# Kernel tuning notes

Hardware: AMD Instinct MI355X
Metric: run time of the kernel (lower is better)

The kernel has to match this reference:

```python
import jax, jax.numpy as jnp
import numpy as np

N_NODES = 100000
N_EDGES = 1600000
N_GRAPHS = 512
IN_DIM = 128
HID = 128


def setup_inputs() -> dict:
    key = jax.random.key(0)
    ks = jax.random.split(key, 8)
    x = jax.random.normal(ks[0], (N_NODES, IN_DIM), dtype=jnp.float32)
    edge_index = jax.random.randint(ks[1], (2, N_EDGES), 0, N_NODES, dtype=jnp.int64)
    batch = jnp.sort(jax.random.randint(ks[2], (N_NODES,), 0, N_GRAPHS, dtype=jnp.int64))
    s1 = 1.0 / np.sqrt(IN_DIM)
    s2 = 1.0 / np.sqrt(HID)
    W1 = jax.random.normal(ks[3], (IN_DIM, HID), dtype=jnp.float32) * s1
    b1 = jnp.zeros((HID,), dtype=jnp.float32)
    W2 = jax.random.normal(ks[4], (HID, HID), dtype=jnp.float32) * s2
    b2 = jnp.zeros((HID,), dtype=jnp.float32)
    Wp = jax.random.normal(ks[5], (HID, 1), dtype=jnp.float32) * s2
    bp = jnp.zeros((1,), dtype=jnp.float32)
    return {"x": x, "edge_index": edge_index, "batch": batch,
            "W1": W1, "b1": b1, "W2": W2, "b2": b2, "Wp": Wp, "bp": bp}


def _gcn_conv(x, W, b, src, dst, deg_inv_sqrt):
    # PyG GCNConv: linear transform, then normalized scatter-add (self-loops
    # already appended to src/dst), then bias.
    h = x @ W                                   # [N, H]
    norm = deg_inv_sqrt[src] * deg_inv_sqrt[dst]  # [E+N]
    msg = h[src] * norm[:, None]                # gather + scale
    out = jax.ops.segment_sum(msg, dst, num_segments=N_NODES)
    return out + b


def reference(x, edge_index, batch, W1, b1, W2, b2, Wp, bp):
    # Add self-loops once; degree (with self-loops) over target nodes.
    si = jnp.arange(N_NODES, dtype=edge_index.dtype)
    src = jnp.concatenate([edge_index[0], si])
    dst = jnp.concatenate([edge_index[1], si])
    ones = jnp.ones(src.shape[0], dtype=x.dtype)
    deg = jax.ops.segment_sum(ones, dst, num_segments=N_NODES)
    deg_inv_sqrt = jnp.where(deg > 0, jax.lax.rsqrt(jnp.maximum(deg, 1.0)), 0.0)

    h = jax.nn.relu(_gcn_conv(x, W1, b1, src, dst, deg_inv_sqrt))  # dropout = identity (eval)
    h = jax.nn.relu(_gcn_conv(h, W2, b2, src, dst, deg_inv_sqrt))

    # global_mean_pool over graph ids
    sums = jax.ops.segment_sum(h, batch, num_segments=N_GRAPHS)
    cnts = jax.ops.segment_sum(jnp.ones(N_NODES, dtype=h.dtype), batch, num_segments=N_GRAPHS)
    pooled = sums / jnp.maximum(cnts, 1.0)[:, None]               # [G, H]

    return (pooled @ Wp + bp).squeeze(-1)                          # [G]
```

## Files before the change

kernel.cpp:

```cpp
#include <hip/hip_runtime.h>
#include <hip/hip_bf16.h>

#define NN 100000
#define NG 512
#define H  128

typedef _Float16 half8 __attribute__((ext_vector_type(8)));
typedef _Float16 half4v __attribute__((ext_vector_type(4)));
typedef float f32x4 __attribute__((ext_vector_type(4)));

__global__ __launch_bounds__(256) void k_hist(const int* __restrict__ dst,
                                              int* __restrict__ deg, int E) {
    int e = blockIdx.x * 256 + threadIdx.x;
    if (e < E) atomicAdd(&deg[dst[e]], 1);
}

__global__ __launch_bounds__(256) void k_scan_block(const int* __restrict__ deg,
                                                    int* __restrict__ rowptr,
                                                    int* __restrict__ bsum, int n) {
    __shared__ int s[256];
    int tid = threadIdx.x;
    int i = blockIdx.x * 256 + tid;
    int v = (i < n) ? deg[i] : 0;
    s[tid] = v;
    __syncthreads();
    #pragma unroll
    for (int off = 1; off < 256; off <<= 1) {
        int t = (tid >= off) ? s[tid - off] : 0;
        __syncthreads();
        s[tid] += t;
        __syncthreads();
    }
    if (i < n) rowptr[i] = s[tid] - v;
    if (tid == 255) bsum[blockIdx.x] = s[255];
}

__global__ __launch_bounds__(512) void k_scan_top(int* __restrict__ bsum, int nb) {
    __shared__ int s[512];
    int tid = threadIdx.x;
    int v = (tid < nb) ? bsum[tid] : 0;
    s[tid] = v;
    __syncthreads();
    #pragma unroll
    for (int off = 1; off < 512; off <<= 1) {
        int t = (tid >= off) ? s[tid - off] : 0;
        __syncthreads();
        s[tid] += t;
        __syncthreads();
    }
    if (tid < nb) bsum[tid] = s[tid] - v;
}

__global__ __launch_bounds__(256) void k_scan_fin(int* __restrict__ rowptr,
                                                  const int* __restrict__ bsum,
                                                  const int* __restrict__ deg,
                                                  int* __restrict__ cursor,
                                                  float* __restrict__ dinv,
                                                  int n, int E) {
    int i = blockIdx.x * 256 + threadIdx.x;
    if (i >= n) return;
    int r = rowptr[i] + bsum[i >> 8];
    rowptr[i] = r;
    cursor[i] = r;
    dinv[i] = rsqrtf((float)deg[i] + 1.0f);
    if (i == 0) rowptr[n] = E;
}

__global__ __launch_bounds__(256) void k_fill(const int* __restrict__ src,
                                              const int* __restrict__ dst,
                                              int* __restrict__ cursor,
                                              int* __restrict__ col, int E) {
    int e = blockIdx.x * 256 + threadIdx.x;
    if (e >= E) return;
    int d = dst[e];
    int pos = atomicAdd(&cursor[d], 1);
    col[pos] = src[e];
}

__global__ __launch_bounds__(256) void k_sortrows(const int* __restrict__ rowptr,
                                                  int* __restrict__ col, int n) {
    int node = blockIdx.x * 4 + (threadIdx.x >> 6);
    int lane = threadIdx.x & 63;
    if (node >= n) return;
    int e0 = rowptr[node], end = rowptr[node + 1];
    int deg = end - e0;
    if (deg <= 1 || deg > 64) return;
    int v = (lane < deg) ? col[e0 + lane] : 0x7fffffff;
    #pragma unroll
    for (int k = 2; k <= 64; k <<= 1) {
        #pragma unroll
        for (int j = k >> 1; j > 0; j >>= 1) {
            int p = __shfl_xor(v, j);
            bool up = ((lane & k) == 0);
            bool keepmin = (((lane & j) == 0) == up);
            v = keepmin ? min(v, p) : max(v, p);
        }
    }
    if (lane < deg) col[e0 + lane] = v;
}

__global__ __launch_bounds__(256) void k_cvt_h(const float* __restrict__ in,
                                               _Float16* __restrict__ out, int n4) {
    int i = blockIdx.x * 256 + threadIdx.x;
    if (i >= n4) return;
    float4 v = ((const float4*)in)[i];
    half4v h;
    h[0] = (_Float16)v.x;
    h[1] = (_Float16)v.y;
    h[2] = (_Float16)v.z;
    h[3] = (_Float16)v.w;
    ((half4v*)out)[i] = h;
}

#define LDA 136
__global__ __launch_bounds__(256) void gemm_mfma(const _Float16* __restrict__ A,
                                                 const float* __restrict__ W,
                                                 const float* __restrict__ scale,
                                                 _Float16* __restrict__ C, int n) {
    __shared__ _Float16 As[64 * LDA];
    __shared__ _Float16 Wt[128 * LDA];
    const int tid = threadIdx.x;
    const int row0 = blockIdx.x * 64;

    #pragma unroll
    for (int i = 0; i < 4; ++i) {
        int f = i * 256 + tid;
        int r = f >> 4, c8 = f & 15;
        int gr = row0 + r;
        half8 v;
        #pragma unroll
        for (int j = 0; j < 8; ++j) v[j] = (_Float16)0.0f;
        if (gr < n) v = ((const half8*)(A + (size_t)gr * H))[c8];
        *((half8*)(As + r * LDA + c8 * 8)) = v;
    }
    #pragma unroll
    for (int i = 0; i < 16; ++i) {
        int f = i * 256 + tid;
        int k = f >> 5, c4 = f & 31;
        float4 v = ((const float4*)(W + (size_t)k * H))[c4];
        Wt[(c4 * 4 + 0) * LDA + k] = (_Float16)v.x;
        Wt[(c4 * 4 + 1) * LDA + k] = (_Float16)v.y;
        Wt[(c4 * 4 + 2) * LDA + k] = (_Float16)v.z;
        Wt[(c4 * 4 + 3) * LDA + k] = (_Float16)v.w;
    }
    __syncthreads();

    const int w = tid >> 6;
    const int lane = tid & 63;
    const int l16 = lane & 15, quad = lane >> 4;
    f32x4 acc[8] = {};
    const _Float16* aBase = As + (w * 16 + l16) * LDA + quad * 8;
    const _Float16* bBase = Wt + l16 * LDA + quad * 8;
    #pragma unroll
    for (int kk = 0; kk < 4; ++kk) {
        half8 af = *((const half8*)(aBase + kk * 32));
        #pragma unroll
        for (int nt = 0; nt < 8; ++nt) {
            half8 bf = *((const half8*)(bBase + nt * 16 * LDA + kk * 32));
            acc[nt] = __builtin_amdgcn_mfma_f32_16x16x32_f16(af, bf, acc[nt], 0, 0, 0);
        }
    }
    #pragma unroll
    for (int r = 0; r < 4; ++r) {
        int R = row0 + w * 16 + quad * 4 + r;
        if (R < n) {
            float sc = scale[R];
            _Float16* crow = C + (size_t)R * H + l16;
            #pragma unroll
            for (int nt = 0; nt < 8; ++nt)
                crow[nt * 16] = (_Float16)(acc[nt][r] * sc);
        }
    }
}

__device__ __forceinline__ void gather_rows_h(const half8* __restrict__ t8,
                                              const int* __restrict__ col,
                                              int node, int e0, int end,
                                              float acc[8]) {
    const int lane = threadIdx.x & 63;
    const int q = lane >> 4;
    const int l16 = lane & 15;
    float a0[8] = {}, a1[8] = {};
    if (q == 0) {
        half8 v = t8[(size_t)node * 16 + l16];
        #pragma unroll
        for (int i = 0; i < 8; ++i) a0[i] = (float)v[i];
    }
    for (int base = e0; base < end; base += 64) {
        int ce = base + lane;
        int cidx = (ce < end) ? col[ce] : 0;
        int m = min(64, end - base);
        int nf = m >> 2;
        int g = 0;
        for (; g + 2 <= nf; g += 2) {
            int s0 = __shfl(cidx, 4 * g + q);
            int s1 = __shfl(cidx, 4 * g + 4 + q);
            half8 v0 = t8[(size_t)s0 * 16 + l16];
            half8 v1 = t8[(size_t)s1 * 16 + l16];
            #pragma unroll
            for (int i = 0; i < 8; ++i) {
                a0[i] += (float)v0[i];
                a1[i] += (float)v1[i];
            }
        }
        if (g < nf) {
            int s0 = __shfl(cidx, 4 * g + q);
            half8 v0 = t8[(size_t)s0 * 16 + l16];
            #pragma unroll
            for (int i = 0; i < 8; ++i) a0[i] += (float)v0[i];
        }
        int tail = m & 3;
        if (tail) {
            int s = __shfl(cidx, 4 * nf + q);
            if (q < tail) {
                half8 v = t8[(size_t)s * 16 + l16];
                #pragma unroll
                for (int i = 0; i < 8; ++i) a0[i] += (float)v[i];
            }
        }
    }
    #pragma unroll
    for (int i = 0; i < 8; ++i) {
        float t = a0[i] + a1[i];
        t += __shfl_xor(t, 16);
        t += __shfl_xor(t, 32);
        acc[i] = t;
    }
}

__global__ __launch_bounds__(256) void k_gather1(const _Float16* __restrict__ tS,
                                                 const int* __restrict__ rowptr,
                                                 const int* __restrict__ col,
                                                 const float* __restrict__ dinv,
                                                 const float* __restrict__ b,
                                                 _Float16* __restrict__ out, int n) {
    int node = blockIdx.x * 4 + (threadIdx.x >> 6);
    int lane = threadIdx.x & 63;
    int q = lane >> 4, l16 = lane & 15;
    if (node >= n) return;
    int e0 = rowptr[node], end = rowptr[node + 1];
    float acc[8];
    gather_rows_h((const half8*)tS, col, node, e0, end, acc);
    if (q == 0) {
        float dn = dinv[node];
        const float4* b4 = (const float4*)b;
        float4 bb0 = b4[2 * l16], bb1 = b4[2 * l16 + 1];
        half8 hv;
        hv[0] = (_Float16)fmaxf(dn * acc[0] + bb0.x, 0.0f);
        hv[1] = (_Float16)fmaxf(dn * acc[1] + bb0.y, 0.0f);
        hv[2] = (_Float16)fmaxf(dn * acc[2] + bb0.z, 0.0f);
        hv[3] = (_Float16)fmaxf(dn * acc[3] + bb0.w, 0.0f);
        hv[4] = (_Float16)fmaxf(dn * acc[4] + bb1.x, 0.0f);
        hv[5] = (_Float16)fmaxf(dn * acc[5] + bb1.y, 0.0f);
        hv[6] = (_Float16)fmaxf(dn * acc[6] + bb1.z, 0.0f);
        hv[7] = (_Float16)fmaxf(dn * acc[7] + bb1.w, 0.0f);
        ((half8*)out)[(size_t)node * 16 + l16] = hv;
    }
}

__global__ __launch_bounds__(256) void k_gather2(const _Float16* __restrict__ tS,
                                                 const int* __restrict__ rowptr,
                                                 const int* __restrict__ col,
                                                 const float* __restrict__ dinv,
                                                 const float* __restrict__ b,
                                                 const float* __restrict__ Wp,
                                                 const int* __restrict__ batch,
                                                 float* __restrict__ pool,
                                                 float* __restrict__ cnt, int n) {
    int node = blockIdx.x * 4 + (threadIdx.x >> 6);
    int lane = threadIdx.x & 63;
    int l16 = lane & 15;
    if (node >= n) return;
    int e0 = rowptr[node], end = rowptr[node + 1];
    float acc[8];
    gather_rows_h((const half8*)tS, col, node, e0, end, acc);
    float dn = dinv[node];
    const float4* b4 = (const float4*)b;
    const float4* w4 = (const float4*)Wp;
    float4 bb0 = b4[2 * l16], bb1 = b4[2 * l16 + 1];
    float4 wp0 = w4[2 * l16], wp1 = w4[2 * l16 + 1];
    float s = fmaxf(dn * acc[0] + bb0.x, 0.0f) * wp0.x +
              fmaxf(dn * acc[1] + bb0.y, 0.0f) * wp0.y +
              fmaxf(dn * acc[2] + bb0.z, 0.0f) * wp0.z +
              fmaxf(dn * acc[3] + bb0.w, 0.0f) * wp0.w +
              fmaxf(dn * acc[4] + bb1.x, 0.0f) * wp1.x +
              fmaxf(dn * acc[5] + bb1.y, 0.0f) * wp1.y +
              fmaxf(dn * acc[6] + bb1.z, 0.0f) * wp1.z +
              fmaxf(dn * acc[7] + bb1.w, 0.0f) * wp1.w;
    s += __shfl_xor(s, 1);
    s += __shfl_xor(s, 2);
    s += __shfl_xor(s, 4);
    s += __shfl_xor(s, 8);
    if (lane == 0) {
        int g = batch[node];
        atomicAdd(&pool[g], s);
        atomicAdd(&cnt[g], 1.0f);
    }
}

__global__ __launch_bounds__(256) void final_out_kernel(const float* __restrict__ pool,
                                                        const float* __restrict__ cnt,
                                                        const float* __restrict__ bp,
                                                        float* __restrict__ out, int g) {
    int i = blockIdx.x * 256 + threadIdx.x;
    if (i < g) out[i] = pool[i] / fmaxf(cnt[i], 1.0f) + bp[0];
}

extern "C" void kernel_launch(void* const* d_in, const int* in_sizes, int n_in,
                              void* d_out, int out_size, void* d_ws, size_t ws_size,
                              hipStream_t stream) {
    const float* x     = (const float*)d_in[0];
    const int*   ei    = (const int*)d_in[1];
    const int*   batch = (const int*)d_in[2];
    const float* W1    = (const float*)d_in[3];
    const float* b1    = (const float*)d_in[4];
    const float* W2    = (const float*)d_in[5];
    const float* b2    = (const float*)d_in[6];
    const float* Wp    = (const float*)d_in[7];
    const float* bp    = (const float*)d_in[8];
    float* out = (float*)d_out;

    const int E = in_sizes[1] / 2;
    const int* src = ei;
    const int* dst = ei + E;

    const size_t BUFH = (size_t)NN * H * sizeof(_Float16);
    const size_t NI  = 401408;
    char* ws = (char*)d_ws;
    size_t off = 0;
    _Float16* tS  = (_Float16*)(ws + off); off += BUFH;
    _Float16* h1  = (_Float16*)(ws + off); off += BUFH;
    _Float16* xh  = (_Float16*)(ws + off); off += BUFH;
    int*   deg    = (int*)  (ws + off); off += NI;
    int*   rowptr = (int*)  (ws + off); off += NI;
    int*   cursor = (int*)  (ws + off); off += NI;
    float* dinv   = (float*)(ws + off); off += NI;
    int*   col    = (int*)  (ws + off); off += ((size_t)E * 4 + 4095) / 4096 * 4096;
    int*   bsum   = (int*)  (ws + off); off += 4096;
    float* pool   = (float*)(ws + off); off += 2048;
    float* cnt    = (float*)(ws + off); off += 2048;

    const int NB = (NN + 255) / 256;

    hipMemsetAsync(deg, 0, NN * sizeof(int), stream);
    hipMemsetAsync(pool, 0, 4096, stream);
    k_hist<<<(E + 255) / 256, 256, 0, stream>>>(dst, deg, E);
    k_scan_block<<<NB, 256, 0, stream>>>(deg, rowptr, bsum, NN);
    k_scan_top<<<1, 512, 0, stream>>>(bsum, NB);
    k_scan_fin<<<NB, 256, 0, stream>>>(rowptr, bsum, deg, cursor, dinv, NN, E);
    k_fill<<<(E + 255) / 256, 256, 0, stream>>>(src, dst, cursor, col, E);
    k_sortrows<<<(NN + 3) / 4, 256, 0, stream>>>(rowptr, col, NN);

    k_cvt_h<<<(NN * 32 + 255) / 256, 256, 0, stream>>>(x, xh, NN * 32);

    gemm_mfma<<<(NN + 63) / 64, 256, 0, stream>>>(xh, W1, dinv, tS, NN);
    k_gather1<<<(NN + 3) / 4, 256, 0, stream>>>(tS, rowptr, col, dinv, b1, h1, NN);

    gemm_mfma<<<(NN + 63) / 64, 256, 0, stream>>>(h1, W2, dinv, tS, NN);
    k_gather2<<<(NN + 3) / 4, 256, 0, stream>>>(tS, rowptr, col, dinv, b2, Wp,
                                                batch, pool, cnt, NN);

    final_out_kernel<<<(NG + 255) / 256, 256, 0, stream>>>(pool, cnt, bp, out, NG);
}
```

Measured before the change: 704.6 us.

## Fuse fill with GEMM1, fuse gather1 with GEMM2, sort rows in-register

Several kernels are merged. The half-precision conversion of x moves into the first GEMM, which also shares one launch with the CSR fill. The second GEMM is fused into the first aggregation kernel through shared memory, so h1 never goes to global memory. The per-row sort pass is dropped and each gather wave sorts its own neighbor list with a bitonic network. Weight transposition is done once up front instead of in every GEMM block. This removes launches and memory round trips, but it adds redundant sorting work in both gathers and lowers gather parallelism to one 64-node block per workgroup, with each wave looping over 16 nodes serially.

```diff
diff --git a/kernel.cpp b/kernel.cpp
--- a/kernel.cpp
+++ b/kernel.cpp
@@ -6,7 +6,6 @@
 #define H  128
 
 typedef _Float16 half8 __attribute__((ext_vector_type(8)));
-typedef _Float16 half4v __attribute__((ext_vector_type(4)));
 typedef float f32x4 __attribute__((ext_vector_type(4)));
 
 __global__ __launch_bounds__(256) void k_hist(const int* __restrict__ dst,
@@ -66,26 +65,72 @@
     if (i == 0) rowptr[n] = E;
 }
 
-__global__ __launch_bounds__(256) void k_fill(const int* __restrict__ src,
-                                              const int* __restrict__ dst,
-                                              int* __restrict__ cursor,
-                                              int* __restrict__ col, int E) {
-    int e = blockIdx.x * 256 + threadIdx.x;
-    if (e >= E) return;
-    int d = dst[e];
-    int pos = atomicAdd(&cursor[d], 1);
-    col[pos] = src[e];
-}
-
-__global__ __launch_bounds__(256) void k_sortrows(const int* __restrict__ rowptr,
-                                                  int* __restrict__ col, int n) {
-    int node = blockIdx.x * 4 + (threadIdx.x >> 6);
-    int lane = threadIdx.x & 63;
-    if (node >= n) return;
-    int e0 = rowptr[node], end = rowptr[node + 1];
-    int deg = end - e0;
-    if (deg <= 1 || deg > 64) return;
-    int v = (lane < deg) ? col[e0 + lane] : 0x7fffffff;
+__global__ __launch_bounds__(256) void k_wprep(const float* __restrict__ W1,
+                                               const float* __restrict__ W2,
+                                               _Float16* __restrict__ Wt1,
+                                               _Float16* __restrict__ Wt2) {
+    int bb = blockIdx.x;
+    const float* W = (bb < 64) ? W1 : W2;
+    _Float16* Wt = (bb < 64) ? Wt1 : Wt2;
+    int i = (bb & 63) * 256 + threadIdx.x;
+    int k = i >> 7, n = i & 127;
+    Wt[n * 128 + k] = (_Float16)W[i];
+}
+
+__global__ __launch_bounds__(256) void k_fill_gemm1(
+        const int* __restrict__ src, const int* __restrict__ dst,
+        int* __restrict__ cursor, int* __restrict__ col, int E, int nfb,
+        const float* __restrict__ x, const _Float16* __restrict__ Wt1,
+        const float* __restrict__ dinv, _Float16* __restrict__ tS, int n) {
+    if ((int)blockIdx.x < nfb) {
+        int e = blockIdx.x * 256 + threadIdx.x;
+        if (e >= E) return;
+        int d = dst[e];
+        int pos = atomicAdd(&cursor[d], 1);
+        col[pos] = src[e];
+        return;
+    }
+    const int row0 = ((int)blockIdx.x - nfb) * 64;
+    const int tid = threadIdx.x;
+    const int w = tid >> 6, lane = tid & 63;
+    const int l16 = lane & 15, quad = lane >> 4;
+    const int Arow = row0 + w * 16 + l16;
+    f32x4 acc[8] = {};
+    #pragma unroll
+    for (int kk = 0; kk < 4; ++kk) {
+        half8 af;
+        if (Arow < n) {
+            const float* ap = x + (size_t)Arow * H + kk * 32 + quad * 8;
+            float4 a0 = ((const float4*)ap)[0];
+            float4 a1 = ((const float4*)ap)[1];
+            af[0] = (_Float16)a0.x; af[1] = (_Float16)a0.y;
+            af[2] = (_Float16)a0.z; af[3] = (_Float16)a0.w;
+            af[4] = (_Float16)a1.x; af[5] = (_Float16)a1.y;
+            af[6] = (_Float16)a1.z; af[7] = (_Float16)a1.w;
+        } else {
+            #pragma unroll
+            for (int j = 0; j < 8; ++j) af[j] = (_Float16)0.0f;
+        }
+        #pragma unroll
+        for (int nt = 0; nt < 8; ++nt) {
+            half8 bf = *((const half8*)(Wt1 + (nt * 16 + l16) * H + kk * 32 + quad * 8));
+            acc[nt] = __builtin_amdgcn_mfma_f32_16x16x32_f16(af, bf, acc[nt], 0, 0, 0);
+        }
+    }
+    #pragma unroll
+    for (int r = 0; r < 4; ++r) {
+        int R = row0 + w * 16 + quad * 4 + r;
+        if (R < n) {
+            float sc = dinv[R];
+            _Float16* crow = tS + (size_t)R * H + l16;
+            #pragma unroll
+            for (int nt = 0; nt < 8; ++nt)
+                crow[nt * 16] = (_Float16)(acc[nt][r] * sc);
+        }
+    }
+}
+
+__device__ __forceinline__ int bitonic64(int v, int lane) {
     #pragma unroll
     for (int k = 2; k <= 64; k <<= 1) {
         #pragma unroll
@@ -96,81 +141,7 @@
             v = keepmin ? min(v, p) : max(v, p);
         }
     }
-    if (lane < deg) col[e0 + lane] = v;
-}
-
-__global__ __launch_bounds__(256) void k_cvt_h(const float* __restrict__ in,
-                                               _Float16* __restrict__ out, int n4) {
-    int i = blockIdx.x * 256 + threadIdx.x;
-    if (i >= n4) return;
-    float4 v = ((const float4*)in)[i];
-    half4v h;
-    h[0] = (_Float16)v.x;
-    h[1] = (_Float16)v.y;
-    h[2] = (_Float16)v.z;
-    h[3] = (_Float16)v.w;
-    ((half4v*)out)[i] = h;
-}
-
-#define LDA 136
-__global__ __launch_bounds__(256) void gemm_mfma(const _Float16* __restrict__ A,
-                                                 const float* __restrict__ W,
-                                                 const float* __restrict__ scale,
-                                                 _Float16* __restrict__ C, int n) {
-    __shared__ _Float16 As[64 * LDA];
-    __shared__ _Float16 Wt[128 * LDA];
-    const int tid = threadIdx.x;
-    const int row0 = blockIdx.x * 64;
-
-    #pragma unroll
-    for (int i = 0; i < 4; ++i) {
-        int f = i * 256 + tid;
-        int r = f >> 4, c8 = f & 15;
-        int gr = row0 + r;
-        half8 v;
-        #pragma unroll
-        for (int j = 0; j < 8; ++j) v[j] = (_Float16)0.0f;
-        if (gr < n) v = ((const half8*)(A + (size_t)gr * H))[c8];
-        *((half8*)(As + r * LDA + c8 * 8)) = v;
-    }
-    #pragma unroll
-    for (int i = 0; i < 16; ++i) {
-        int f = i * 256 + tid;
-        int k = f >> 5, c4 = f & 31;
-        float4 v = ((const float4*)(W + (size_t)k * H))[c4];
-        Wt[(c4 * 4 + 0) * LDA + k] = (_Float16)v.x;
-        Wt[(c4 * 4 + 1) * LDA + k] = (_Float16)v.y;
-        Wt[(c4 * 4 + 2) * LDA + k] = (_Float16)v.z;
-        Wt[(c4 * 4 + 3) * LDA + k] = (_Float16)v.w;
-    }
-    __syncthreads();
-
-    const int w = tid >> 6;
-    const int lane = tid & 63;
-    const int l16 = lane & 15, quad = lane >> 4;
-    f32x4 acc[8] = {};
-    const _Float16* aBase = As + (w * 16 + l16) * LDA + quad * 8;
-    const _Float16* bBase = Wt + l16 * LDA + quad * 8;
-    #pragma unroll
-    for (int kk = 0; kk < 4; ++kk) {
-        half8 af = *((const half8*)(aBase + kk * 32));
-        #pragma unroll
-        for (int nt = 0; nt < 8; ++nt) {
-            half8 bf = *((const half8*)(bBase + nt * 16 * LDA + kk * 32));
-            acc[nt] = __builtin_amdgcn_mfma_f32_16x16x32_f16(af, bf, acc[nt], 0, 0, 0);
-        }
-    }
-    #pragma unroll
-    for (int r = 0; r < 4; ++r) {
-        int R = row0 + w * 16 + quad * 4 + r;
-        if (R < n) {
-            float sc = scale[R];
-            _Float16* crow = C + (size_t)R * H + l16;
-            #pragma unroll
-            for (int nt = 0; nt < 8; ++nt)
-                crow[nt * 16] = (_Float16)(acc[nt][r] * sc);
-        }
-    }
+    return v;
 }
 
 __device__ __forceinline__ void gather_rows_h(const half8* __restrict__ t8,
@@ -186,9 +157,11 @@
         #pragma unroll
         for (int i = 0; i < 8; ++i) a0[i] = (float)v[i];
     }
+    const bool small = (end - e0) <= 64;
     for (int base = e0; base < end; base += 64) {
         int ce = base + lane;
-        int cidx = (ce < end) ? col[ce] : 0;
+        int cidx = (ce < end) ? col[ce] : 0x7fffffff;
+        if (small) cidx = bitonic64(cidx, lane);
         int m = min(64, end - base);
         int nf = m >> 2;
         int g = 0;
@@ -228,33 +201,67 @@
     }
 }
 
-__global__ __launch_bounds__(256) void k_gather1(const _Float16* __restrict__ tS,
-                                                 const int* __restrict__ rowptr,
-                                                 const int* __restrict__ col,
-                                                 const float* __restrict__ dinv,
-                                                 const float* __restrict__ b,
-                                                 _Float16* __restrict__ out, int n) {
-    int node = blockIdx.x * 4 + (threadIdx.x >> 6);
-    int lane = threadIdx.x & 63;
-    int q = lane >> 4, l16 = lane & 15;
-    if (node >= n) return;
-    int e0 = rowptr[node], end = rowptr[node + 1];
-    float acc[8];
-    gather_rows_h((const half8*)tS, col, node, e0, end, acc);
-    if (q == 0) {
-        float dn = dinv[node];
-        const float4* b4 = (const float4*)b;
-        float4 bb0 = b4[2 * l16], bb1 = b4[2 * l16 + 1];
+#define LDA 136
+__global__ __launch_bounds__(256) void k_gather1f(const _Float16* __restrict__ tS,
+                                                  const int* __restrict__ rowptr,
+                                                  const int* __restrict__ col,
+                                                  const float* __restrict__ dinv,
+                                                  const float* __restrict__ b,
+                                                  const _Float16* __restrict__ Wt2,
+                                                  _Float16* __restrict__ tS2, int n) {
+    __shared__ _Float16 As[64 * LDA];
+    const int tid = threadIdx.x;
+    const int w = tid >> 6, lane = tid & 63;
+    const int q = lane >> 4, l16 = lane & 15, quad = lane >> 4;
+    const int node0 = blockIdx.x * 64;
+    const float4* b4 = (const float4*)b;
+    float4 bb0 = b4[2 * l16], bb1 = b4[2 * l16 + 1];
+
+    for (int i = 0; i < 16; ++i) {
+        int node = node0 + w * 16 + i;
         half8 hv;
-        hv[0] = (_Float16)fmaxf(dn * acc[0] + bb0.x, 0.0f);
-        hv[1] = (_Float16)fmaxf(dn * acc[1] + bb0.y, 0.0f);
-        hv[2] = (_Float16)fmaxf(dn * acc[2] + bb0.z, 0.0f);
-        hv[3] = (_Float16)fmaxf(dn * acc[3] + bb0.w, 0.0f);
-        hv[4] = (_Float16)fmaxf(dn * acc[4] + bb1.x, 0.0f);
-        hv[5] = (_Float16)fmaxf(dn * acc[5] + bb1.y, 0.0f);
-        hv[6] = (_Float16)fmaxf(dn * acc[6] + bb1.z, 0.0f);
-        hv[7] = (_Float16)fmaxf(dn * acc[7] + bb1.w, 0.0f);
-        ((half8*)out)[(size_t)node * 16 + l16] = hv;
+        #pragma unroll
+        for (int j = 0; j < 8; ++j) hv[j] = (_Float16)0.0f;
+        if (node < n) {
+            int e0 = rowptr[node], end = rowptr[node + 1];
+            float acc[8];
+            gather_rows_h((const half8*)tS, col, node, e0, end, acc);
+            float dn = dinv[node];
+            hv[0] = (_Float16)fmaxf(dn * acc[0] + bb0.x, 0.0f);
+            hv[1] = (_Float16)fmaxf(dn * acc[1] + bb0.y, 0.0f);
+            hv[2] = (_Float16)fmaxf(dn * acc[2] + bb0.z, 0.0f);
+            hv[3] = (_Float16)fmaxf(dn * acc[3] + bb0.w, 0.0f);
+            hv[4] = (_Float16)fmaxf(dn * acc[4] + bb1.x, 0.0f);
+            hv[5] = (_Float16)fmaxf(dn * acc[5] + bb1.y, 0.0f);
+            hv[6] = (_Float16)fmaxf(dn * acc[6] + bb1.z, 0.0f);
+            hv[7] = (_Float16)fmaxf(dn * acc[7] + bb1.w, 0.0f);
+        }
+        if (q == 0)
+            *((half8*)(As + (w * 16 + i) * LDA + l16 * 8)) = hv;
+    }
+    __syncthreads();
+
+    f32x4 acc2[8] = {};
+    const _Float16* aBase = As + (w * 16 + l16) * LDA + quad * 8;
+    #pragma unroll
+    for (int kk = 0; kk < 4; ++kk) {
+        half8 af = *((const half8*)(aBase + kk * 32));
+        #pragma unroll
+        for (int nt = 0; nt < 8; ++nt) {
+            half8 bf = *((const half8*)(Wt2 + (nt * 16 + l16) * H + kk * 32 + quad * 8));
+            acc2[nt] = __builtin_amdgcn_mfma_f32_16x16x32_f16(af, bf, acc2[nt], 0, 0, 0);
+        }
+    }
+    #pragma unroll
+    for (int r = 0; r < 4; ++r) {
+        int R = node0 + w * 16 + quad * 4 + r;
+        if (R < n) {
+            float sc = dinv[R];
+            _Float16* crow = tS2 + (size_t)R * H + l16;
+            #pragma unroll
+            for (int nt = 0; nt < 8; ++nt)
+                crow[nt * 16] = (_Float16)(acc2[nt][r] * sc);
+        }
     }
 }
 
@@ -325,39 +332,40 @@
     const int* dst = ei + E;
 
     const size_t BUFH = (size_t)NN * H * sizeof(_Float16);
-    const size_t NI  = 401408;
+    const size_t NI   = 401408;
     char* ws = (char*)d_ws;
     size_t off = 0;
-    _Float16* tS  = (_Float16*)(ws + off); off += BUFH;
-    _Float16* h1  = (_Float16*)(ws + off); off += BUFH;
-    _Float16* xh  = (_Float16*)(ws + off); off += BUFH;
-    int*   deg    = (int*)  (ws + off); off += NI;
-    int*   rowptr = (int*)  (ws + off); off += NI;
-    int*   cursor = (int*)  (ws + off); off += NI;
-    float* dinv   = (float*)(ws + off); off += NI;
-    int*   col    = (int*)  (ws + off); off += ((size_t)E * 4 + 4095) / 4096 * 4096;
-    int*   bsum   = (int*)  (ws + off); off += 4096;
-    float* pool   = (float*)(ws + off); off += 2048;
-    float* cnt    = (float*)(ws + off); off += 2048;
-
-    const int NB = (NN + 255) / 256;
+    _Float16* tS   = (_Float16*)(ws + off); off += BUFH;
+    _Float16* tS2  = (_Float16*)(ws + off); off += BUFH;
+    int*      deg  = (int*)     (ws + off); off += NI;
+    int*   rowptr  = (int*)     (ws + off); off += NI;
+    int*   cursor  = (int*)     (ws + off); off += NI;
+    float*    dinv = (float*)   (ws + off); off += NI;
+    int*      col  = (int*)     (ws + off); off += ((size_t)E * 4 + 4095) / 4096 * 4096;
+    _Float16* Wt1  = (_Float16*)(ws + off); off += 32768;
+    _Float16* Wt2  = (_Float16*)(ws + off); off += 32768;
+    int*      bsum = (int*)     (ws + off); off += 4096;
+    float*    pool = (float*)   (ws + off); off += 2048;
+    float*    cnt  = (float*)   (ws + off); off += 2048;
+
+    const int NB  = (NN + 255) / 256;
+    const int NFB = (E + 255) / 256;
+    const int NGB = (NN + 63) / 64;
 
     hipMemsetAsync(deg, 0, NN * sizeof(int), stream);
     hipMemsetAsync(pool, 0, 4096, stream);
-    k_hist<<<(E + 255) / 256, 256, 0, stream>>>(dst, deg, E);
+    k_wprep<<<128, 256, 0, stream>>>(W1, W2, Wt1, Wt2);
+    k_hist<<<NFB, 256, 0, stream>>>(dst, deg, E);
     k_scan_block<<<NB, 256, 0, stream>>>(deg, rowptr, bsum, NN);
     k_scan_top<<<1, 512, 0, stream>>>(bsum, NB);
     k_scan_fin<<<NB, 256, 0, stream>>>(rowptr, bsum, deg, cursor, dinv, NN, E);
-    k_fill<<<(E + 255) / 256, 256, 0, stream>>>(src, dst, cursor, col, E);
-    k_sortrows<<<(NN + 3) / 4, 256, 0, stream>>>(rowptr, col, NN);
-
-    k_cvt_h<<<(NN * 32 + 255) / 256, 256, 0, stream>>>(x, xh, NN * 32);
-
-    gemm_mfma<<<(NN + 63) / 64, 256, 0, stream>>>(xh, W1, dinv, tS, NN);
-    k_gather1<<<(NN + 3) / 4, 256, 0, stream>>>(tS, rowptr, col, dinv, b1, h1, NN);
-
-    gemm_mfma<<<(NN + 63) / 64, 256, 0, stream>>>(h1, W2, dinv, tS, NN);
-    k_gather2<<<(NN + 3) / 4, 256, 0, stream>>>(tS, rowptr, col, dinv, b2, Wp,
+
+    k_fill_gemm1<<<NFB + NGB, 256, 0, stream>>>(src, dst, cursor, col, E, NFB,
+                                                x, Wt1, dinv, tS, NN);
+
+    k_gather1f<<<NGB, 256, 0, stream>>>(tS, rowptr, col, dinv, b1, Wt2, tS2, NN);
+
+    k_gather2<<<(NN + 3) / 4, 256, 0, stream>>>(tS2, rowptr, col, dinv, b2, Wp,
                                                 batch, pool, cnt, NN);
 
     final_out_kernel<<<(NG + 255) / 256, 256, 0, stream>>>(pool, cnt, bp, out, NG);
```

Result: slower. 732.4 us (+3.9%).
